# Performance work log

Hardware: AMD Instinct MI355X
Metric: run time of the kernel (lower is better)

Reference implementation:

```python
import jax, jax.numpy as jnp
import numpy as np

B, L, C, NH = 512, 129, 512, 8
TAU = 1.0


def layer_norm(x, g, b, eps=1e-5):
    m = x.mean(-1, keepdims=True)
    v = x.var(-1, keepdims=True)
    return (x - m) / jnp.sqrt(v + eps) * g + b


def attn_pool(tokens, query, in_w, in_b, out_w, out_b, ln_g, ln_b):
    # single-query multi-head attention pooling (nn.MultiheadAttention, batch_first)
    Bn, Ln, Cn = tokens.shape
    dh = Cn // NH
    Wq, Wk, Wv = jnp.split(in_w, 3, axis=0)
    bq, bk, bv = jnp.split(in_b, 3)
    q = (query[0, 0] @ Wq.T + bq).reshape(NH, dh)           # (H, dh), shared across batch
    k = (tokens @ Wk.T + bk).reshape(Bn, Ln, NH, dh)
    v = (tokens @ Wv.T + bv).reshape(Bn, Ln, NH, dh)
    scale = 1.0 / jnp.sqrt(jnp.asarray(dh, tokens.dtype))
    scores = jnp.einsum('hd,blhd->bhl', q, k) * scale       # (B, H, L)
    w = jax.nn.softmax(scores, axis=-1)
    out = jnp.einsum('bhl,blhd->bhd', w, v).reshape(Bn, Cn)
    out = out @ out_w.T + out_b
    return layer_norm(out, ln_g, ln_b)


def entropy(feat):
    fa = jnp.abs(feat) + 1e-8
    p = fa / fa.sum(-1, keepdims=True)
    return -(p * jnp.log(p + 1e-8)).sum(-1)


def setup_inputs() -> dict:
    key = jax.random.key(0)
    ks = jax.random.split(key, 20)
    s = C ** -0.5
    inp = {
        'rgb_tokens': jax.random.normal(ks[0], (B, L, C), jnp.float32),
        'nir_tokens': jax.random.normal(ks[1], (B, L, C), jnp.float32),
        'tir_tokens': jax.random.normal(ks[2], (B, L, C), jnp.float32),
        'rgb_query': s * jax.random.normal(ks[3], (1, 1, C), jnp.float32),
        'nir_query': s * jax.random.normal(ks[4], (1, 1, C), jnp.float32),
        'tir_query': s * jax.random.normal(ks[5], (1, 1, C), jnp.float32),
        'in_proj_w': 0.02 * jax.random.normal(ks[6], (3 * C, C), jnp.float32),
        'in_proj_b': jnp.zeros((3 * C,), jnp.float32),
        'out_proj_w': 0.02 * jax.random.normal(ks[7], (C, C), jnp.float32),
        'out_proj_b': jnp.zeros((C,), jnp.float32),
        'attn_ln_g': jnp.ones((C,), jnp.float32),
        'attn_ln_b': jnp.zeros((C,), jnp.float32),
        'ent_w': 0.02 * jax.random.normal(ks[8], (C, C), jnp.float32),
        'ent_b': jnp.zeros((C,), jnp.float32),
        'gate_w1': 0.02 * jax.random.normal(ks[9], (C, 3 * C), jnp.float32),
        'gate_b1': jnp.zeros((C,), jnp.float32),
        'gate_ln_g': jnp.ones((C,), jnp.float32),
        'gate_ln_b': jnp.zeros((C,), jnp.float32),
        'gate_w2': 0.02 * jax.random.normal(ks[10], (3, C), jnp.float32),
        'gate_b2': jnp.zeros((3,), jnp.float32),
        'alpha_raw': jnp.asarray(0.5, jnp.float32),
        'enh_w': 0.02 * jax.random.normal(ks[11], (C, C), jnp.float32),
        'enh_b': jnp.zeros((C,), jnp.float32),
        'enh_ln_g': jnp.ones((C,), jnp.float32),
        'enh_ln_b': jnp.zeros((C,), jnp.float32),
    }
    return inp


def reference(rgb_tokens, nir_tokens, tir_tokens, rgb_query, nir_query, tir_query,
              in_proj_w, in_proj_b, out_proj_w, out_proj_b, attn_ln_g, attn_ln_b,
              ent_w, ent_b, gate_w1, gate_b1, gate_ln_g, gate_ln_b, gate_w2, gate_b2,
              alpha_raw, enh_w, enh_b, enh_ln_g, enh_ln_b):
    ap = lambda t, q: attn_pool(t, q, in_proj_w, in_proj_b, out_proj_w, out_proj_b, attn_ln_g, attn_ln_b)
    h_rgb, h_nir, h_tir = ap(rgb_tokens, rgb_query), ap(nir_tokens, nir_query), ap(tir_tokens, tir_query)
    H_r, H_n, H_t = entropy(h_rgb), entropy(h_nir), entropy(h_tir)
    z = lambda h: (h @ ent_w.T + ent_b).mean(-1)
    scores = jnp.stack([z(h_rgb) * jnp.exp(-H_r / TAU),
                        z(h_nir) * jnp.exp(-H_n / TAU),
                        z(h_tir) * jnp.exp(-H_t / TAU)], axis=-1)   # (B, 3)
    ew = jax.nn.softmax(scores, axis=-1)
    h_entropy = ew[:, 0:1] * h_rgb + ew[:, 1:2] * h_nir + ew[:, 2:3] * h_tir
    h_concat = jnp.concatenate([h_rgb, h_nir, h_tir], axis=-1)      # (B, 3C)
    g = jax.nn.relu(layer_norm(h_concat @ gate_w1.T + gate_b1, gate_ln_g, gate_ln_b))
    gates = jax.nn.sigmoid(g @ gate_w2.T + gate_b2)                  # (B, 3)
    h_importance = gates[:, 0:1] * h_rgb + gates[:, 1:2] * h_nir + gates[:, 2:3] * h_tir
    alpha = jax.nn.sigmoid(alpha_raw)
    h_fused = alpha * h_entropy + (1.0 - alpha) * h_importance
    h_enh = layer_norm(h_fused @ enh_w.T + enh_b, enh_ln_g, enh_ln_b)
    return jnp.concatenate([h_rgb + h_enh, h_nir + h_enh, h_tir + h_enh], axis=-1)  # (B, 3C)
```

## Files before the change

kernel.cpp:

```cpp
#include <hip/hip_runtime.h>
#include <cstdint>

#define WS_U      0
#define WS_C0     12288
#define WS_ENTBM  12312
#define WS_ENTP   12320
#define WS_P      16416
#define WS_OUT2   WS_P
#define WS_GPRE   (WS_P + 786432)
#define WS_HFUSED (WS_P + 1572864)
#define WS_ENHPRE (WS_P + 1835008)
#define WS_VOUT   (WS_P + 6291456)
#define WS_HCAT   (WS_VOUT + 786432)
#define WS_H      (WS_HCAT + 786432)
#define WS_Z      (WS_H + 1536)

__device__ __forceinline__ float blk_sum4(float v, float* red, int lane, int wave) {
#pragma unroll
  for (int off = 32; off; off >>= 1) v += __shfl_xor(v, off);
  __syncthreads();
  if (lane == 0) red[wave] = v;
  __syncthreads();
  return red[0] + red[1] + red[2] + red[3];
}

__global__ __launch_bounds__(256) void prep_kernel(
    const float* __restrict__ qrgb, const float* __restrict__ qnir, const float* __restrict__ qtir,
    const float* __restrict__ inw, const float* __restrict__ inb,
    const float* __restrict__ entw, const float* __restrict__ entb,
    float* __restrict__ ws)
{
  const int m = blockIdx.x, h = blockIdx.y;
  const int tid = threadIdx.x, lane = tid & 63, wave = tid >> 6;
  __shared__ float qvl[64];
  __shared__ float red[4];

  if (m == 3) {
    const float* base = entw + (size_t)h * 64 * 512;
    float acc0 = 0.f, acc1 = 0.f;
#pragma unroll 8
    for (int r = 0; r < 64; r++) {
      acc0 += base[(size_t)r * 512 + tid];
      acc1 += base[(size_t)r * 512 + tid + 256];
    }
    ws[WS_ENTP + h * 512 + tid] = acc0;
    ws[WS_ENTP + h * 512 + tid + 256] = acc1;
    return;
  }

  const float* qry = (m == 0) ? qrgb : (m == 1) ? qnir : qtir;
  float4 q0 = *(const float4*)(qry + 4 * lane);
  float4 q1 = *(const float4*)(qry + 256 + 4 * lane);
#pragma unroll 4
  for (int dd = 0; dd < 16; dd++) {
    const int d = wave * 16 + dd;
    const float* wr = inw + (size_t)(h * 64 + d) * 512;
    float4 w0 = *(const float4*)(wr + 4 * lane);
    float4 w1 = *(const float4*)(wr + 256 + 4 * lane);
    float p = w0.x * q0.x + w0.y * q0.y + w0.z * q0.z + w0.w * q0.w
            + w1.x * q1.x + w1.y * q1.y + w1.z * q1.z + w1.w * q1.w;
#pragma unroll
    for (int off = 32; off; off >>= 1) p += __shfl_xor(p, off);
    if (lane == 0) qvl[d] = p + inb[h * 64 + d];
  }
  __syncthreads();
  float acc0 = 0.f, acc1 = 0.f;
  const float* wk = inw + (size_t)(512 + h * 64) * 512;
#pragma unroll 8
  for (int d = 0; d < 64; d++) {
    float qq = qvl[d];
    acc0 = fmaf(qq, wk[(size_t)d * 512 + tid], acc0);
    acc1 = fmaf(qq, wk[(size_t)d * 512 + tid + 256], acc1);
  }
  ws[WS_U + m * 4096 + h * 512 + tid] = 0.125f * acc0;
  ws[WS_U + m * 4096 + h * 512 + tid + 256] = 0.125f * acc1;
  if (m == 0 && h == 0) {
    float v = entb[tid] + entb[tid + 256];
    float s = blk_sum4(v, red, lane, wave);
    if (tid == 0) ws[WS_ENTBM] = s * (1.f / 512.f);
  }
}

__global__ __launch_bounds__(256, 2) void attn_pool_kernel(
    const float* __restrict__ trgb, const float* __restrict__ tnir, const float* __restrict__ ttir,
    const float* __restrict__ ws, float* __restrict__ Pout)
{
  const int b = blockIdx.x, m = blockIdx.y;
  const int tid = threadIdx.x, lane = tid & 63, wave = tid >> 6;
  const float* tok = ((m == 0) ? trgb : (m == 1) ? tnir : ttir) + (size_t)b * 129 * 512;
  const float* u = ws + WS_U + m * 4096;

  __shared__ float lacc[4][4][512];
  __shared__ float lstat[4][16];
  __shared__ float tsh[4][8];

  float4 u0[8], u1[8];
#pragma unroll
  for (int h = 0; h < 8; h++) {
    u0[h] = *(const float4*)(u + h * 512 + 4 * lane);
    u1[h] = *(const float4*)(u + h * 512 + 256 + 4 * lane);
  }
  const int s0 = lane & 1, s1 = (lane >> 1) & 1, s2 = (lane >> 2) & 1;
  const int hidx = ((lane & 1) << 2) | (lane & 2) | ((lane >> 2) & 1);

  float acc[8][8];
  float mh[8], sh[8];
#pragma unroll
  for (int h = 0; h < 8; h++) {
    mh[h] = 0.f; sh[h] = 0.f;
#pragma unroll
    for (int j = 0; j < 8; j++) acc[h][j] = 0.f;
  }

  auto process_row = [&](const float4 a, const float4 c) {
    float p[8];
#pragma unroll
    for (int h = 0; h < 8; h++)
      p[h] = a.x * u0[h].x + a.y * u0[h].y + a.z * u0[h].z + a.w * u0[h].w
           + c.x * u1[h].x + c.y * u1[h].y + c.z * u1[h].z + c.w * u1[h].w;
    float q0 = (s0 ? p[4] : p[0]) + __shfl_xor(s0 ? p[0] : p[4], 1);
    float q1 = (s0 ? p[5] : p[1]) + __shfl_xor(s0 ? p[1] : p[5], 1);
    float q2 = (s0 ? p[6] : p[2]) + __shfl_xor(s0 ? p[2] : p[6], 1);
    float q3 = (s0 ? p[7] : p[3]) + __shfl_xor(s0 ? p[3] : p[7], 1);
    float r0 = (s1 ? q2 : q0) + __shfl_xor(s1 ? q0 : q2, 2);
    float r1 = (s1 ? q3 : q1) + __shfl_xor(s1 ? q1 : q3, 2);
    float t  = (s2 ? r1 : r0) + __shfl_xor(s2 ? r0 : r1, 4);
    t += __shfl_xor(t, 8);
    t += __shfl_xor(t, 16);
    t += __shfl_xor(t, 32);
    if (lane < 8) tsh[wave][hidx] = t;
#pragma unroll
    for (int h = 0; h < 8; h++) {
      float tv = tsh[wave][h];
      if (tv > mh[h] + 8.0f) {
        float scl = __expf(mh[h] - tv);
        sh[h] *= scl;
#pragma unroll
        for (int j = 0; j < 8; j++) acc[h][j] *= scl;
        mh[h] = tv;
      }
      float w = __expf(tv - mh[h]);
      sh[h] += w;
      acc[h][0] = fmaf(w, a.x, acc[h][0]);
      acc[h][1] = fmaf(w, a.y, acc[h][1]);
      acc[h][2] = fmaf(w, a.z, acc[h][2]);
      acc[h][3] = fmaf(w, a.w, acc[h][3]);
      acc[h][4] = fmaf(w, c.x, acc[h][4]);
      acc[h][5] = fmaf(w, c.y, acc[h][5]);
      acc[h][6] = fmaf(w, c.z, acc[h][6]);
      acc[h][7] = fmaf(w, c.w, acc[h][7]);
    }
  };

  const int nrows = (wave == 0) ? 33 : 32;
  const float* r0p = tok + (size_t)wave * 512;
  float4 a0 = *(const float4*)(r0p + 4 * lane);
  float4 c0 = *(const float4*)(r0p + 256 + 4 * lane);
  const float* r1p = tok + (size_t)(wave + 4) * 512;
  float4 a1 = *(const float4*)(r1p + 4 * lane);
  float4 c1 = *(const float4*)(r1p + 256 + 4 * lane);
  for (int i = 0; i + 2 < nrows; i++) {
    const float* np = tok + (size_t)(wave + 4 * (i + 2)) * 512;
    float4 na = *(const float4*)(np + 4 * lane);
    float4 nc = *(const float4*)(np + 256 + 4 * lane);
    process_row(a0, c0);
    a0 = a1; c0 = c1;
    a1 = na; c1 = nc;
  }
  process_row(a0, c0);
  process_row(a1, c1);

  if (lane == 0) {
#pragma unroll
    for (int h = 0; h < 8; h++) {
      lstat[wave][h] = mh[h];
      lstat[wave][8 + h] = sh[h];
    }
  }
  __syncthreads();
  float fw[4][8];
#pragma unroll
  for (int h = 0; h < 8; h++) {
    float m0 = lstat[0][h], m1 = lstat[1][h], m2 = lstat[2][h], m3 = lstat[3][h];
    float Mx = fmaxf(fmaxf(m0, m1), fmaxf(m2, m3));
    float f0 = __expf(m0 - Mx), f1 = __expf(m1 - Mx);
    float f2 = __expf(m2 - Mx), f3 = __expf(m3 - Mx);
    float S = lstat[0][8 + h] * f0 + lstat[1][8 + h] * f1
            + lstat[2][8 + h] * f2 + lstat[3][8 + h] * f3;
    float is = 1.f / S;
    fw[0][h] = f0 * is; fw[1][h] = f1 * is; fw[2][h] = f2 * is; fw[3][h] = f3 * is;
  }
  float* po = Pout + (size_t)(m * 512 + b) * 4096 + 2 * tid;
#pragma unroll
  for (int hb = 0; hb < 8; hb += 4) {
    if (hb) __syncthreads();
#pragma unroll
    for (int hh = 0; hh < 4; hh++) {
      const int h = hb + hh;
      *(float4*)&lacc[wave][hh][4 * lane] =
          make_float4(acc[h][0], acc[h][1], acc[h][2], acc[h][3]);
      *(float4*)&lacc[wave][hh][256 + 4 * lane] =
          make_float4(acc[h][4], acc[h][5], acc[h][6], acc[h][7]);
    }
    __syncthreads();
#pragma unroll
    for (int hh = 0; hh < 4; hh++) {
      const int h = hb + hh;
      float2 x0 = *(const float2*)&lacc[0][hh][2 * tid];
      float2 x1 = *(const float2*)&lacc[1][hh][2 * tid];
      float2 x2 = *(const float2*)&lacc[2][hh][2 * tid];
      float2 x3 = *(const float2*)&lacc[3][hh][2 * tid];
      float ox = x0.x * fw[0][h] + x1.x * fw[1][h] + x2.x * fw[2][h] + x3.x * fw[3][h];
      float oy = x0.y * fw[0][h] + x1.y * fw[1][h] + x2.y * fw[2][h] + x3.y * fw[3][h];
      *(float2*)(po + h * 512) = make_float2(ox, oy);
    }
  }
}

__global__ __launch_bounds__(256) void gemm_bt_kernel(
    const float* __restrict__ A, const float* __restrict__ B,
    const float* __restrict__ bias, float* __restrict__ C,
    int K, int lda, int ldb, int ldc,
    long sA, long sB, long sC, int sBias, int addBias)
{
  A += (long)blockIdx.z * sA;
  B += (long)blockIdx.z * sB;
  C += (long)blockIdx.z * sC;
  const float* bp = bias + (long)blockIdx.z * sBias;
  __shared__ float As[32][68];
  __shared__ float Bs[32][68];
  const int tid = threadIdx.x;
  const int tx = tid & 15, ty = tid >> 4;
  const int rowL = tid >> 3;
  const int colv = (tid & 7) << 2;
  const int m0 = blockIdx.x * 64, n0 = blockIdx.y * 64;
  float acc[4][4] = {};
  for (int k0 = 0; k0 < K; k0 += 32) {
#pragma unroll
    for (int it = 0; it < 2; it++) {
      const int r = rowL + it * 32;
      float4 v = *(const float4*)(A + (size_t)(m0 + r) * lda + k0 + colv);
      As[colv + 0][r] = v.x; As[colv + 1][r] = v.y; As[colv + 2][r] = v.z; As[colv + 3][r] = v.w;
      float4 w = *(const float4*)(B + (size_t)(n0 + r) * ldb + k0 + colv);
      Bs[colv + 0][r] = w.x; Bs[colv + 1][r] = w.y; Bs[colv + 2][r] = w.z; Bs[colv + 3][r] = w.w;
    }
    __syncthreads();
#pragma unroll
    for (int k = 0; k < 32; k++) {
      float4 a4 = *(const float4*)&As[k][ty * 4];
      float4 b4 = *(const float4*)&Bs[k][tx * 4];
      acc[0][0] += a4.x * b4.x; acc[0][1] += a4.x * b4.y; acc[0][2] += a4.x * b4.z; acc[0][3] += a4.x * b4.w;
      acc[1][0] += a4.y * b4.x; acc[1][1] += a4.y * b4.y; acc[1][2] += a4.y * b4.z; acc[1][3] += a4.y * b4.w;
      acc[2][0] += a4.z * b4.x; acc[2][1] += a4.z * b4.y; acc[2][2] += a4.z * b4.z; acc[2][3] += a4.z * b4.w;
      acc[3][0] += a4.w * b4.x; acc[3][1] += a4.w * b4.y; acc[3][2] += a4.w * b4.z; acc[3][3] += a4.w * b4.w;
    }
    __syncthreads();
  }
  float4 bv = make_float4(0.f, 0.f, 0.f, 0.f);
  if (addBias) bv = *(const float4*)(bp + n0 + tx * 4);
#pragma unroll
  for (int i = 0; i < 4; i++) {
    float4 o;
    o.x = acc[i][0] + bv.x; o.y = acc[i][1] + bv.y;
    o.z = acc[i][2] + bv.z; o.w = acc[i][3] + bv.w;
    *(float4*)(C + (size_t)(m0 + ty * 4 + i) * ldc + n0 + tx * 4) = o;
  }
}

__global__ __launch_bounds__(256) void ln_ent_kernel(
    const float* __restrict__ out2,
    const float* __restrict__ lng, const float* __restrict__ lnb,
    const float* __restrict__ ws, float* __restrict__ hcat,
    float* __restrict__ Hout, float* __restrict__ zout)
{
  const int r = blockIdx.x;
  const int mod = r >> 9, b = r & 511;
  const int tid = threadIdx.x, lane = tid & 63, wave = tid >> 6;
  __shared__ float red[4];
  const float* x = out2 + (size_t)r * 512;
  float2 v = *(const float2*)(x + 2 * tid);
  float s = blk_sum4(v.x + v.y, red, lane, wave);
  float sq = blk_sum4(v.x * v.x + v.y * v.y, red, lane, wave);
  float mean = s * (1.f / 512.f);
  float var = sq * (1.f / 512.f) - mean * mean;
  float rstd = rsqrtf(var + 1e-5f);
  float2 g = *(const float2*)(lng + 2 * tid);
  float2 bb = *(const float2*)(lnb + 2 * tid);
  float h0 = (v.x - mean) * rstd * g.x + bb.x;
  float h1 = (v.y - mean) * rstd * g.y + bb.y;
  *(float2*)(hcat + (size_t)b * 1536 + mod * 512 + 2 * tid) = make_float2(h0, h1);
  float2 ep = make_float2(0.f, 0.f);
#pragma unroll
  for (int j = 0; j < 8; j++) {
    float2 t = *(const float2*)(ws + WS_ENTP + j * 512 + 2 * tid);
    ep.x += t.x; ep.y += t.y;
  }
  ep.x *= (1.f / 512.f); ep.y *= (1.f / 512.f);
  float fa0 = fabsf(h0) + 1e-8f, fa1 = fabsf(h1) + 1e-8f;
  float S = blk_sum4(fa0 + fa1, red, lane, wave);
  float zz = blk_sum4(h0 * ep.x + h1 * ep.y, red, lane, wave);
  float invS = 1.f / S;
  float p0 = fa0 * invS, p1 = fa1 * invS;
  float t = blk_sum4(p0 * logf(p0 + 1e-8f) + p1 * logf(p1 + 1e-8f), red, lane, wave);
  if (tid == 0) {
    Hout[mod * 512 + b] = -t;
    zout[mod * 512 + b] = zz + ws[WS_ENTBM];
  }
}

__global__ __launch_bounds__(256) void gate_fuse_kernel(
    const float* __restrict__ gpre, const float* __restrict__ glng, const float* __restrict__ glnb,
    const float* __restrict__ gw2, const float* __restrict__ gb2, const float* __restrict__ gb1,
    const float* __restrict__ araw, const float* __restrict__ hcat,
    const float* __restrict__ H, const float* __restrict__ z,
    float* __restrict__ hfused)
{
  const int b = blockIdx.x;
  const int tid = threadIdx.x, lane = tid & 63, wave = tid >> 6;
  __shared__ float red[4];
  float2 v;
  {
    float2 p0 = *(const float2*)(gpre + (size_t)b * 512 + 2 * tid);
    float2 p1 = *(const float2*)(gpre + 262144 + (size_t)b * 512 + 2 * tid);
    float2 p2 = *(const float2*)(gpre + 524288 + (size_t)b * 512 + 2 * tid);
    float2 bi = *(const float2*)(gb1 + 2 * tid);
    v.x = p0.x + p1.x + p2.x + bi.x;
    v.y = p0.y + p1.y + p2.y + bi.y;
  }
  float s = blk_sum4(v.x + v.y, red, lane, wave);
  float sq = blk_sum4(v.x * v.x + v.y * v.y, red, lane, wave);
  float mean = s * (1.f / 512.f), var = sq * (1.f / 512.f) - mean * mean;
  float rstd = rsqrtf(var + 1e-5f);
  float2 g = *(const float2*)(glng + 2 * tid);
  float2 bb = *(const float2*)(glnb + 2 * tid);
  float g0 = fmaxf((v.x - mean) * rstd * g.x + bb.x, 0.f);
  float g1 = fmaxf((v.y - mean) * rstd * g.y + bb.y, 0.f);
  float d0 = blk_sum4(g0 * gw2[2 * tid] + g1 * gw2[2 * tid + 1], red, lane, wave);
  float d1 = blk_sum4(g0 * gw2[512 + 2 * tid] + g1 * gw2[512 + 2 * tid + 1], red, lane, wave);
  float d2 = blk_sum4(g0 * gw2[1024 + 2 * tid] + g1 * gw2[1024 + 2 * tid + 1], red, lane, wave);
  float ga0 = 1.f / (1.f + __expf(-(d0 + gb2[0])));
  float ga1 = 1.f / (1.f + __expf(-(d1 + gb2[1])));
  float ga2 = 1.f / (1.f + __expf(-(d2 + gb2[2])));
  float sc0 = z[b] * __expf(-H[b]);
  float sc1 = z[512 + b] * __expf(-H[512 + b]);
  float sc2 = z[1024 + b] * __expf(-H[1024 + b]);
  float mxs = fmaxf(sc0, fmaxf(sc1, sc2));
  float e0 = __expf(sc0 - mxs), e1 = __expf(sc1 - mxs), e2 = __expf(sc2 - mxs);
  float inv = 1.f / (e0 + e1 + e2);
  e0 *= inv; e1 *= inv; e2 *= inv;
  float alpha = 1.f / (1.f + __expf(-araw[0]));
  const float* hb = hcat + (size_t)b * 1536 + 2 * tid;
  float2 hr = *(const float2*)hb;
  float2 hn = *(const float2*)(hb + 512);
  float2 ht = *(const float2*)(hb + 1024);
  float2 o;
  o.x = alpha * (e0 * hr.x + e1 * hn.x + e2 * ht.x)
      + (1.f - alpha) * (ga0 * hr.x + ga1 * hn.x + ga2 * ht.x);
  o.y = alpha * (e0 * hr.y + e1 * hn.y + e2 * ht.y)
      + (1.f - alpha) * (ga0 * hr.y + ga1 * hn.y + ga2 * ht.y);
  *(float2*)(hfused + (size_t)b * 512 + 2 * tid) = o;
}

__global__ __launch_bounds__(256) void final_out_kernel(
    const float* __restrict__ epre, const float* __restrict__ enb,
    const float* __restrict__ elng, const float* __restrict__ elnb,
    const float* __restrict__ hcat, float* __restrict__ out)
{
  const int b = blockIdx.x;
  const int tid = threadIdx.x, lane = tid & 63, wave = tid >> 6;
  __shared__ float red[4];
  float2 v;
  {
    float2 p0 = *(const float2*)(epre + (size_t)b * 512 + 2 * tid);
    float2 p1 = *(const float2*)(epre + 262144 + (size_t)b * 512 + 2 * tid);
    float2 bi = *(const float2*)(enb + 2 * tid);
    v.x = p0.x + p1.x + bi.x;
    v.y = p0.y + p1.y + bi.y;
  }
  float s = blk_sum4(v.x + v.y, red, lane, wave);
  float sq = blk_sum4(v.x * v.x + v.y * v.y, red, lane, wave);
  float mean = s * (1.f / 512.f), var = sq * (1.f / 512.f) - mean * mean;
  float rstd = rsqrtf(var + 1e-5f);
  float2 g = *(const float2*)(elng + 2 * tid);
  float2 bb = *(const float2*)(elnb + 2 * tid);
  float e0 = (v.x - mean) * rstd * g.x + bb.x;
  float e1 = (v.y - mean) * rstd * g.y + bb.y;
  const float* hb = hcat + (size_t)b * 1536 + 2 * tid;
  float* ob = out + (size_t)b * 1536 + 2 * tid;
#pragma unroll
  for (int mm = 0; mm < 3; mm++) {
    float2 hv = *(const float2*)(hb + mm * 512);
    *(float2*)(ob + mm * 512) = make_float2(hv.x + e0, hv.y + e1);
  }
}

extern "C" void kernel_launch(void* const* d_in, const int* in_sizes, int n_in,
                              void* d_out, int out_size, void* d_ws, size_t ws_size,
                              hipStream_t stream)
{
  const float* trgb = (const float*)d_in[0];
  const float* tnir = (const float*)d_in[1];
  const float* ttir = (const float*)d_in[2];
  const float* qrgb = (const float*)d_in[3];
  const float* qnir = (const float*)d_in[4];
  const float* qtir = (const float*)d_in[5];
  const float* inw  = (const float*)d_in[6];
  const float* inb  = (const float*)d_in[7];
  const float* outw = (const float*)d_in[8];
  const float* outb = (const float*)d_in[9];
  const float* alng = (const float*)d_in[10];
  const float* alnb = (const float*)d_in[11];
  const float* entw = (const float*)d_in[12];
  const float* entb = (const float*)d_in[13];
  const float* gw1  = (const float*)d_in[14];
  const float* gb1  = (const float*)d_in[15];
  const float* glng = (const float*)d_in[16];
  const float* glnb = (const float*)d_in[17];
  const float* gw2  = (const float*)d_in[18];
  const float* gb2  = (const float*)d_in[19];
  const float* araw = (const float*)d_in[20];
  const float* enw  = (const float*)d_in[21];
  const float* enb  = (const float*)d_in[22];
  const float* elng = (const float*)d_in[23];
  const float* elnb = (const float*)d_in[24];
  float* ws = (float*)d_ws;
  float* out = (float*)d_out;

  hipLaunchKernelGGL(prep_kernel, dim3(4, 8), dim3(256), 0, stream,
                     qrgb, qnir, qtir, inw, inb, entw, entb, ws);
  hipLaunchKernelGGL(attn_pool_kernel, dim3(512, 3), dim3(256), 0, stream,
                     trgb, tnir, ttir, ws, ws + WS_P);
  hipLaunchKernelGGL(gemm_bt_kernel, dim3(24, 1, 8), dim3(256), 0, stream,
                     ws + WS_P, inw + (size_t)1024 * 512, inb + 1024, ws + WS_VOUT,
                     512, 4096, 512, 512,
                     (long)512, (long)64 * 512, (long)64, 64, 1);
  hipLaunchKernelGGL(gemm_bt_kernel, dim3(24, 8, 1), dim3(256), 0, stream,
                     ws + WS_VOUT, outw, outb, ws + WS_OUT2,
                     512, 512, 512, 512, 0L, 0L, 0L, 0, 1);
  hipLaunchKernelGGL(ln_ent_kernel, dim3(1536), dim3(256), 0, stream,
                     ws + WS_OUT2, alng, alnb, ws, ws + WS_HCAT, ws + WS_H, ws + WS_Z);
  hipLaunchKernelGGL(gemm_bt_kernel, dim3(8, 8, 3), dim3(256), 0, stream,
                     ws + WS_HCAT, gw1, gb1, ws + WS_GPRE,
                     512, 1536, 1536, 512,
                     (long)512, (long)512, (long)262144, 0, 0);
  hipLaunchKernelGGL(gate_fuse_kernel, dim3(512), dim3(256), 0, stream,
                     ws + WS_GPRE, glng, glnb, gw2, gb2, gb1, araw,
                     ws + WS_HCAT, ws + WS_H, ws + WS_Z, ws + WS_HFUSED);
  hipLaunchKernelGGL(gemm_bt_kernel, dim3(8, 8, 2), dim3(256), 0, stream,
                     ws + WS_HFUSED, enw, enb, ws + WS_ENHPRE,
                     256, 512, 512, 512,
                     (long)256, (long)256, (long)262144, 0, 0);
  hipLaunchKernelGGL(final_out_kernel, dim3(512), dim3(256), 0, stream,
                     ws + WS_ENHPRE, enb, elng, elnb, ws + WS_HCAT, out);
}
```

Baseline: 266.7 us.

## Process two token rows per step with packed FP32 FMA in attention pooling

Measured after the change: 311.5 us. +16.8%, slower.

```diff
diff --git a/kernel.cpp b/kernel.cpp
--- a/kernel.cpp
+++ b/kernel.cpp
@@ -15,6 +15,12 @@
 #define WS_H      (WS_HCAT + 786432)
 #define WS_Z      (WS_H + 1536)
 
+typedef float v2f __attribute__((ext_vector_type(2)));
+
+__device__ __forceinline__ void pkfma(v2f& d, v2f a, v2f b) {
+  asm("v_pk_fma_f32 %0, %1, %2, %0" : "+v"(d) : "v"(a), "v"(b));
+}
+
 __device__ __forceinline__ float blk_sum4(float v, float* red, int lane, int wave) {
 #pragma unroll
   for (int off = 32; off; off >>= 1) v += __shfl_xor(v, off);
@@ -92,83 +98,119 @@
 
   __shared__ float lacc[4][4][512];
   __shared__ float lstat[4][16];
-  __shared__ float tsh[4][8];
-
-  float4 u0[8], u1[8];
+  __shared__ float4 tsh4[4][8];
+
+  v2f u2[8][4];
 #pragma unroll
   for (int h = 0; h < 8; h++) {
-    u0[h] = *(const float4*)(u + h * 512 + 4 * lane);
-    u1[h] = *(const float4*)(u + h * 512 + 256 + 4 * lane);
+    float4 a = *(const float4*)(u + h * 512 + 4 * lane);
+    float4 c = *(const float4*)(u + h * 512 + 256 + 4 * lane);
+    u2[h][0] = v2f{a.x, a.y}; u2[h][1] = v2f{a.z, a.w};
+    u2[h][2] = v2f{c.x, c.y}; u2[h][3] = v2f{c.z, c.w};
   }
   const int s0 = lane & 1, s1 = (lane >> 1) & 1, s2 = (lane >> 2) & 1;
-  const int hidx = ((lane & 1) << 2) | (lane & 2) | ((lane >> 2) & 1);
-
-  float acc[8][8];
+  const int hidx = (s0 << 2) | (s1 << 1) | s2;
+
+  v2f acc2[8][4];
   float mh[8], sh[8];
 #pragma unroll
   for (int h = 0; h < 8; h++) {
     mh[h] = 0.f; sh[h] = 0.f;
 #pragma unroll
-    for (int j = 0; j < 8; j++) acc[h][j] = 0.f;
-  }
-
-  auto process_row = [&](const float4 a, const float4 c) {
-    float p[8];
-#pragma unroll
-    for (int h = 0; h < 8; h++)
-      p[h] = a.x * u0[h].x + a.y * u0[h].y + a.z * u0[h].z + a.w * u0[h].w
-           + c.x * u1[h].x + c.y * u1[h].y + c.z * u1[h].z + c.w * u1[h].w;
-    float q0 = (s0 ? p[4] : p[0]) + __shfl_xor(s0 ? p[0] : p[4], 1);
-    float q1 = (s0 ? p[5] : p[1]) + __shfl_xor(s0 ? p[1] : p[5], 1);
-    float q2 = (s0 ? p[6] : p[2]) + __shfl_xor(s0 ? p[2] : p[6], 1);
-    float q3 = (s0 ? p[7] : p[3]) + __shfl_xor(s0 ? p[3] : p[7], 1);
-    float r0 = (s1 ? q2 : q0) + __shfl_xor(s1 ? q0 : q2, 2);
-    float r1 = (s1 ? q3 : q1) + __shfl_xor(s1 ? q1 : q3, 2);
-    float t  = (s2 ? r1 : r0) + __shfl_xor(s2 ? r0 : r1, 4);
-    t += __shfl_xor(t, 8);
-    t += __shfl_xor(t, 16);
-    t += __shfl_xor(t, 32);
-    if (lane < 8) tsh[wave][hidx] = t;
+    for (int j = 0; j < 4; j++) acc2[h][j] = v2f{0.f, 0.f};
+  }
+
+  auto loadrow = [&](int l, v2f (&r)[4]) {
+    const float* rp = tok + (size_t)l * 512;
+    float4 a = *(const float4*)(rp + 4 * lane);
+    float4 c = *(const float4*)(rp + 256 + 4 * lane);
+    r[0] = v2f{a.x, a.y}; r[1] = v2f{a.z, a.w};
+    r[2] = v2f{c.x, c.y}; r[3] = v2f{c.z, c.w};
+  };
+
+  auto body = [&](const v2f (&rA)[4], const v2f (&rB)[4], bool ZB) {
+    float pA[8], pB[8];
 #pragma unroll
     for (int h = 0; h < 8; h++) {
-      float tv = tsh[wave][h];
-      if (tv > mh[h] + 8.0f) {
-        float scl = __expf(mh[h] - tv);
+      v2f dA = v2f{0.f, 0.f}, dB = v2f{0.f, 0.f};
+      pkfma(dA, rA[0], u2[h][0]); pkfma(dB, rB[0], u2[h][0]);
+      pkfma(dA, rA[1], u2[h][1]); pkfma(dB, rB[1], u2[h][1]);
+      pkfma(dA, rA[2], u2[h][2]); pkfma(dB, rB[2], u2[h][2]);
+      pkfma(dA, rA[3], u2[h][3]); pkfma(dB, rB[3], u2[h][3]);
+      pA[h] = dA.x + dA.y; pB[h] = dB.x + dB.y;
+    }
+    float aq0 = (s0 ? pA[4] : pA[0]) + __shfl_xor(s0 ? pA[0] : pA[4], 1);
+    float bq0 = (s0 ? pB[4] : pB[0]) + __shfl_xor(s0 ? pB[0] : pB[4], 1);
+    float aq1 = (s0 ? pA[5] : pA[1]) + __shfl_xor(s0 ? pA[1] : pA[5], 1);
+    float bq1 = (s0 ? pB[5] : pB[1]) + __shfl_xor(s0 ? pB[1] : pB[5], 1);
+    float aq2 = (s0 ? pA[6] : pA[2]) + __shfl_xor(s0 ? pA[2] : pA[6], 1);
+    float bq2 = (s0 ? pB[6] : pB[2]) + __shfl_xor(s0 ? pB[2] : pB[6], 1);
+    float aq3 = (s0 ? pA[7] : pA[3]) + __shfl_xor(s0 ? pA[3] : pA[7], 1);
+    float bq3 = (s0 ? pB[7] : pB[3]) + __shfl_xor(s0 ? pB[3] : pB[7], 1);
+    float ar0 = (s1 ? aq2 : aq0) + __shfl_xor(s1 ? aq0 : aq2, 2);
+    float br0 = (s1 ? bq2 : bq0) + __shfl_xor(s1 ? bq0 : bq2, 2);
+    float ar1 = (s1 ? aq3 : aq1) + __shfl_xor(s1 ? aq1 : aq3, 2);
+    float br1 = (s1 ? bq3 : bq1) + __shfl_xor(s1 ? bq1 : bq3, 2);
+    float tA = (s2 ? ar1 : ar0) + __shfl_xor(s2 ? ar0 : ar1, 4);
+    float tB = (s2 ? br1 : br0) + __shfl_xor(s2 ? br0 : br1, 4);
+    tA += __shfl_xor(tA, 8);  tB += __shfl_xor(tB, 8);
+    tA += __shfl_xor(tA, 16); tB += __shfl_xor(tB, 16);
+    tA += __shfl_xor(tA, 32); tB += __shfl_xor(tB, 32);
+
+    float msel = s0 ? (s1 ? (s2 ? mh[7] : mh[6]) : (s2 ? mh[5] : mh[4]))
+                    : (s1 ? (s2 ? mh[3] : mh[2]) : (s2 ? mh[1] : mh[0]));
+    float mA = (tA > msel + 8.f) ? tA : msel;
+    float wAo = __expf(tA - mA);
+    float mB = mA, wBo = 0.f;
+    if (!ZB) {
+      mB = (tB > mA + 8.f) ? tB : mA;
+      wBo = __expf(tB - mB);
+    }
+    if (lane < 8) tsh4[wave][hidx] = make_float4(wAo, mA, wBo, mB);
+#pragma unroll
+    for (int h = 0; h < 8; h++) {
+      float4 wm = tsh4[wave][h];
+      if (wm.w > mh[h]) {
+        float scl = __expf(mh[h] - wm.w);
         sh[h] *= scl;
 #pragma unroll
-        for (int j = 0; j < 8; j++) acc[h][j] *= scl;
-        mh[h] = tv;
+        for (int j = 0; j < 4; j++) { acc2[h][j].x *= scl; acc2[h][j].y *= scl; }
+        wm.x *= __expf(wm.y - wm.w);
+        mh[h] = wm.w;
       }
-      float w = __expf(tv - mh[h]);
-      sh[h] += w;
-      acc[h][0] = fmaf(w, a.x, acc[h][0]);
-      acc[h][1] = fmaf(w, a.y, acc[h][1]);
-      acc[h][2] = fmaf(w, a.z, acc[h][2]);
-      acc[h][3] = fmaf(w, a.w, acc[h][3]);
-      acc[h][4] = fmaf(w, c.x, acc[h][4]);
-      acc[h][5] = fmaf(w, c.y, acc[h][5]);
-      acc[h][6] = fmaf(w, c.z, acc[h][6]);
-      acc[h][7] = fmaf(w, c.w, acc[h][7]);
+      sh[h] += wm.x + wm.z;
+      v2f wa = v2f{wm.x, wm.x};
+      pkfma(acc2[h][0], wa, rA[0]);
+      pkfma(acc2[h][1], wa, rA[1]);
+      pkfma(acc2[h][2], wa, rA[2]);
+      pkfma(acc2[h][3], wa, rA[3]);
+      if (!ZB) {
+        v2f wb = v2f{wm.z, wm.z};
+        pkfma(acc2[h][0], wb, rB[0]);
+        pkfma(acc2[h][1], wb, rB[1]);
+        pkfma(acc2[h][2], wb, rB[2]);
+        pkfma(acc2[h][3], wb, rB[3]);
+      }
     }
   };
 
-  const int nrows = (wave == 0) ? 33 : 32;
-  const float* r0p = tok + (size_t)wave * 512;
-  float4 a0 = *(const float4*)(r0p + 4 * lane);
-  float4 c0 = *(const float4*)(r0p + 256 + 4 * lane);
-  const float* r1p = tok + (size_t)(wave + 4) * 512;
-  float4 a1 = *(const float4*)(r1p + 4 * lane);
-  float4 c1 = *(const float4*)(r1p + 256 + 4 * lane);
-  for (int i = 0; i + 2 < nrows; i++) {
-    const float* np = tok + (size_t)(wave + 4 * (i + 2)) * 512;
-    float4 na = *(const float4*)(np + 4 * lane);
-    float4 nc = *(const float4*)(np + 256 + 4 * lane);
-    process_row(a0, c0);
-    a0 = a1; c0 = c1;
-    a1 = na; c1 = nc;
-  }
-  process_row(a0, c0);
-  process_row(a1, c1);
+  v2f rA[4], rB[4], nA[4], nB[4];
+  loadrow(wave, rA);
+  loadrow(wave + 4, rB);
+#pragma unroll 2
+  for (int it = 0; it < 15; ++it) {
+    const int ln = wave + 8 * (it + 1);
+    loadrow(ln, nA);
+    loadrow(ln + 4, nB);
+    body(rA, rB, false);
+#pragma unroll
+    for (int j = 0; j < 4; j++) { rA[j] = nA[j]; rB[j] = nB[j]; }
+  }
+  body(rA, rB, false);
+  if (wave == 0) {
+    loadrow(128, rA);
+    body(rA, rA, true);
+  }
 
   if (lane == 0) {
 #pragma unroll
@@ -198,9 +240,9 @@
     for (int hh = 0; hh < 4; hh++) {
       const int h = hb + hh;
       *(float4*)&lacc[wave][hh][4 * lane] =
-          make_float4(acc[h][0], acc[h][1], acc[h][2], acc[h][3]);
+          make_float4(acc2[h][0].x, acc2[h][0].y, acc2[h][1].x, acc2[h][1].y);
       *(float4*)&lacc[wave][hh][256 + 4 * lane] =
-          make_float4(acc[h][4], acc[h][5], acc[h][6], acc[h][7]);
+          make_float4(acc2[h][2].x, acc2[h][2].y, acc2[h][3].x, acc2[h][3].y);
     }
     __syncthreads();
 #pragma unroll
```
